# Performance work log

Measured on AMD Instinct MI355X. Metric: run time of the kernel, lower is better.

Reference implementation:

```python
import jax, jax.numpy as jnp
import numpy as np

B, N, NEMBED, E, H = 4, 256, 10000, 63, 128
D = E + 1  # feature dim after concat = 64


def _lin(key, fan_in, fan_out):
    k1, k2 = jax.random.split(key)
    bound = 1.0 / np.sqrt(fan_in)
    W = jax.random.uniform(k1, (fan_in, fan_out), jnp.float32, -bound, bound)
    b = jax.random.uniform(k2, (fan_out,), jnp.float32, -bound, bound)
    return W, b


def setup_inputs() -> dict:
    key = jax.random.key(0)
    ks = jax.random.split(key, 9)
    xcat = jax.random.randint(ks[0], (B, N), 0, NEMBED, dtype=jnp.int64)
    xfeat = jax.random.normal(ks[1], (B, N), dtype=jnp.float32)
    emb = jax.random.normal(ks[2], (NEMBED, E), dtype=jnp.float32)
    W1, b1 = _lin(ks[3], D, H)
    W2, b2 = _lin(ks[4], H, H)
    W3, b3 = _lin(ks[5], H, H)
    D1, c1 = _lin(ks[6], H, H)
    D2, c2 = _lin(ks[7], H, H)
    D3, c3 = _lin(ks[8], H, 1)
    return {"xcat": xcat, "xfeat": xfeat, "emb": emb,
            "W1": W1, "b1": b1, "W2": W2, "b2": b2, "W3": W3, "b3": b3,
            "D1": D1, "c1": c1, "D2": D2, "c2": c2, "D3": D3, "c3": c3}


def reference(xcat, xfeat, emb, W1, b1, W2, b2, W3, b3, D1, c1, D2, c2, D3, c3):
    # embed + concat scalar feature -> [B, N, D]
    x = jnp.concatenate([emb[xcat], xfeat[..., None]], axis=-1)
    # pairwise outer product over the set dim -> [B, N, N, D]
    # (original: einsum 'bid,bjd->bdij' then permute(0,2,3,1) == 'bid,bjd->bijd')
    p = jnp.einsum('bid,bjd->bijd', x, x)
    # per-pair 3-layer MLP (enc)
    h = jnp.maximum(p @ W1 + b1, 0.0)
    h = jnp.maximum(h @ W2 + b2, 0.0)
    h = h @ W3 + b3
    # relu -> mean pool over (i, j) -> relu; dropout is identity in eval
    h = jnp.maximum(h, 0.0)
    h = jnp.mean(h, axis=(1, 2))  # [B, H]
    h = jnp.maximum(h, 0.0)
    # dec MLP -> [B, 1]
    h = jnp.maximum(h @ D1 + c1, 0.0)
    h = jnp.maximum(h @ D2 + c2, 0.0)
    return h @ D3 + c3
```

## Files before the change

### kernel.cpp

```cpp
#include <hip/hip_runtime.h>
#include <hip/hip_bf16.h>


#define NB 4
#define NN 256
#define HD 128
#define TPB 257

typedef __attribute__((ext_vector_type(8))) short bf16x8;
typedef __attribute__((ext_vector_type(4))) float f32x4;

__device__ __forceinline__ unsigned rne2(float a, float b) {
    unsigned ua = __builtin_bit_cast(unsigned, a);
    unsigned ub = __builtin_bit_cast(unsigned, b);
    ua = ua + 0x7fff + ((ua >> 16) & 1);
    ub = ub + 0x7fff + ((ub >> 16) & 1);
    return (ua >> 16) | (ub & 0xffff0000u);
}

__device__ __forceinline__ short f2bf(float f) {
    unsigned u = __builtin_bit_cast(unsigned, f);
    u = (u + 0x7fff + ((u >> 16) & 1)) >> 16;
    return (short)u;
}

__device__ __forceinline__ void tri_ij(int t, int& i, int& j) {
    j = (int)((sqrtf(8.0f * (float)t + 1.0f) - 1.0f) * 0.5f);
    while (((j + 1) * (j + 2) >> 1) <= t) ++j;
    while (((j * (j + 1)) >> 1) > t) --j;
    i = t - ((j * (j + 1)) >> 1);
}

__device__ __forceinline__ void pack_w_nat(const float* __restrict__ W, short* __restrict__ pw,
                                           int KQ, int u) {
    int l  = u & 63;
    int kq = (u >> 6) % KQ;
    int mt = (u >> 6) / KQ;
    int q = l >> 4, m = l & 15;
    int c = mt * 16 + m;
#pragma unroll
    for (int j = 0; j < 8; ++j) {
        int k = kq * 32 + q * 8 + j;
        pw[u * 8 + j] = f2bf(W[k * 128 + c]);
    }
}

__device__ __forceinline__ void pack_w_perm(const float* __restrict__ W, short* __restrict__ pw,
                                            int u) {
    int l  = u & 63;
    int kq = (u >> 6) & 3;
    int mt = (u >> 6) >> 2;
    int q = l >> 4, m = l & 15;
    int c = mt * 16 + m;
#pragma unroll
    for (int j = 0; j < 8; ++j) {
        int k = 32 * kq + 16 * (j >> 2) + 4 * q + (j & 3);
        pw[u * 8 + j] = f2bf(W[k * 128 + c]);
    }
}

__global__ void prep_kernel(const int* __restrict__ xcat,
                            const float* __restrict__ xfeat,
                            const float* __restrict__ emb,
                            const float* __restrict__ W1,
                            const float* __restrict__ W2,
                            const float* __restrict__ W3,
                            float* __restrict__ x,
                            short* __restrict__ pw1,
                            short* __restrict__ pw2,
                            short* __restrict__ pw3)
{
    int bid = blockIdx.x;
    int tid = threadIdx.x;
    if (bid < 256) {
        int f = bid * 256 + tid;
        int d = f & 63;
        int nn = f >> 6;
        float v;
        if (d < 63) v = emb[xcat[nn] * 63 + d];
        else        v = xfeat[nn];
        x[f] = v;
    } else if (bid < 260) {
        pack_w_nat(W1, pw1, 2, (bid - 256) * 256 + tid);
    } else if (bid < 268) {
        pack_w_perm(W2, pw2, (bid - 260) * 256 + tid);
    } else {
        pack_w_perm(W3, pw3, (bid - 268) * 256 + tid);
    }
}

__global__ __launch_bounds__(256, 3) void pair_mlp(
    const float* __restrict__ x,
    const short* __restrict__ pw1, const float* __restrict__ b1,
    const short* __restrict__ pw2, const float* __restrict__ b2,
    const short* __restrict__ pw3, const float* __restrict__ b3,
    float* __restrict__ partialOut)
{
    __shared__ float smPart[4][HD];

    const int tid = threadIdx.x;
    const int w = __builtin_amdgcn_readfirstlane(tid >> 6);
    const int l = tid & 63;
    const int q = l >> 4;
    const int n = l & 15;
    const int b = blockIdx.y;
    const float* xb = x + (b << 14);

    const int p0 = blockIdx.x * 128 + w * 32 + n;
    int i0, j0, i1, j1;
    tri_ij(p0, i0, j0);
    tri_ij(p0 + 16, i1, j1);
    const float wp0 = (i0 == j0) ? 1.0f : 2.0f;
    const float wp1 = (i1 == j1) ? 1.0f : 2.0f;

    bf16x8 bp[2][2];
    {
        const float* xi[2] = {xb + (i0 << 6), xb + (i1 << 6)};
        const float* xj[2] = {xb + (j0 << 6), xb + (j1 << 6)};
#pragma unroll
        for (int nt = 0; nt < 2; ++nt)
#pragma unroll
            for (int kq = 0; kq < 2; ++kq) {
                int dd = kq * 32 + q * 8;
                float4 A0 = *(const float4*)(xi[nt] + dd);
                float4 A1 = *(const float4*)(xi[nt] + dd + 4);
                float4 B0 = *(const float4*)(xj[nt] + dd);
                float4 B1 = *(const float4*)(xj[nt] + dd + 4);
                uint4 s;
                s.x = rne2(A0.x * B0.x, A0.y * B0.y);
                s.y = rne2(A0.z * B0.z, A0.w * B0.w);
                s.z = rne2(A1.x * B1.x, A1.y * B1.y);
                s.w = rne2(A1.z * B1.z, A1.w * B1.w);
                bp[nt][kq] = __builtin_bit_cast(bf16x8, s);
            }
    }

    f32x4 acc[8][2];
    unsigned pk[2][8][2];

#pragma unroll
    for (int mt = 0; mt < 8; ++mt) {
        float4 bv = *(const float4*)(b1 + mt * 16 + q * 4);
        f32x4 init = {bv.x, bv.y, bv.z, bv.w};
        acc[mt][0] = init; acc[mt][1] = init;
    }
#pragma unroll
    for (int kq = 0; kq < 2; ++kq)
#pragma unroll
        for (int mt = 0; mt < 8; ++mt) {
            bf16x8 afr = *(const bf16x8*)(pw1 + (((mt * 2 + kq) * 64 + l) << 3));
            acc[mt][0] = __builtin_amdgcn_mfma_f32_16x16x32_bf16(afr, bp[0][kq], acc[mt][0], 0, 0, 0);
            acc[mt][1] = __builtin_amdgcn_mfma_f32_16x16x32_bf16(afr, bp[1][kq], acc[mt][1], 0, 0, 0);
        }

#pragma unroll
    for (int nt = 0; nt < 2; ++nt)
#pragma unroll
        for (int mt = 0; mt < 8; ++mt) {
            pk[nt][mt][0] = rne2(fmaxf(acc[mt][nt][0], 0.f), fmaxf(acc[mt][nt][1], 0.f));
            pk[nt][mt][1] = rne2(fmaxf(acc[mt][nt][2], 0.f), fmaxf(acc[mt][nt][3], 0.f));
        }

#pragma unroll
    for (int mt = 0; mt < 8; ++mt) {
        float4 bv = *(const float4*)(b2 + mt * 16 + q * 4);
        f32x4 init = {bv.x, bv.y, bv.z, bv.w};
        acc[mt][0] = init; acc[mt][1] = init;
    }
#pragma unroll
    for (int kq = 0; kq < 4; ++kq) {
        uint4 u0 = {pk[0][2 * kq][0], pk[0][2 * kq][1], pk[0][2 * kq + 1][0], pk[0][2 * kq + 1][1]};
        uint4 u1 = {pk[1][2 * kq][0], pk[1][2 * kq][1], pk[1][2 * kq + 1][0], pk[1][2 * kq + 1][1]};
        bf16x8 bf0 = __builtin_bit_cast(bf16x8, u0);
        bf16x8 bf1 = __builtin_bit_cast(bf16x8, u1);
#pragma unroll
        for (int mt = 0; mt < 8; ++mt) {
            bf16x8 afr = *(const bf16x8*)(pw2 + (((mt * 4 + kq) * 64 + l) << 3));
            acc[mt][0] = __builtin_amdgcn_mfma_f32_16x16x32_bf16(afr, bf0, acc[mt][0], 0, 0, 0);
            acc[mt][1] = __builtin_amdgcn_mfma_f32_16x16x32_bf16(afr, bf1, acc[mt][1], 0, 0, 0);
        }
    }

#pragma unroll
    for (int nt = 0; nt < 2; ++nt)
#pragma unroll
        for (int mt = 0; mt < 8; ++mt) {
            pk[nt][mt][0] = rne2(fmaxf(acc[mt][nt][0], 0.f), fmaxf(acc[mt][nt][1], 0.f));
            pk[nt][mt][1] = rne2(fmaxf(acc[mt][nt][2], 0.f), fmaxf(acc[mt][nt][3], 0.f));
        }

#pragma unroll
    for (int mt = 0; mt < 8; ++mt) {
        float4 bv = *(const float4*)(b3 + mt * 16 + q * 4);
        f32x4 init = {bv.x, bv.y, bv.z, bv.w};
        acc[mt][0] = init; acc[mt][1] = init;
    }
#pragma unroll
    for (int kq = 0; kq < 4; ++kq) {
        uint4 u0 = {pk[0][2 * kq][0], pk[0][2 * kq][1], pk[0][2 * kq + 1][0], pk[0][2 * kq + 1][1]};
        uint4 u1 = {pk[1][2 * kq][0], pk[1][2 * kq][1], pk[1][2 * kq + 1][0], pk[1][2 * kq + 1][1]};
        bf16x8 bf0 = __builtin_bit_cast(bf16x8, u0);
        bf16x8 bf1 = __builtin_bit_cast(bf16x8, u1);
#pragma unroll
        for (int mt = 0; mt < 8; ++mt) {
            bf16x8 afr = *(const bf16x8*)(pw3 + (((mt * 4 + kq) * 64 + l) << 3));
            acc[mt][0] = __builtin_amdgcn_mfma_f32_16x16x32_bf16(afr, bf0, acc[mt][0], 0, 0, 0);
            acc[mt][1] = __builtin_amdgcn_mfma_f32_16x16x32_bf16(afr, bf1, acc[mt][1], 0, 0, 0);
        }
    }

#pragma unroll
    for (int mt = 0; mt < 8; ++mt) {
        float vs[4];
#pragma unroll
        for (int r = 0; r < 4; ++r) {
            float v = wp0 * fmaxf(acc[mt][0][r], 0.f) + wp1 * fmaxf(acc[mt][1][r], 0.f);
            v += __shfl_xor(v, 1, 64);
            v += __shfl_xor(v, 2, 64);
            v += __shfl_xor(v, 4, 64);
            v += __shfl_xor(v, 8, 64);
            vs[r] = v;
        }
        if (n == 0) {
            float4 o = {vs[0], vs[1], vs[2], vs[3]};
            *(float4*)(&smPart[w][mt * 16 + q * 4]) = o;
        }
    }
    __syncthreads();

    if (tid < HD) {
        float v = (smPart[0][tid] + smPart[1][tid]) + (smPart[2][tid] + smPart[3][tid]);
        partialOut[(b * TPB + blockIdx.x) * HD + tid] = v;
    }
}

__global__ __launch_bounds__(1024) void reduce_decode(
    const float* __restrict__ partial,
    const float* __restrict__ D1, const float* __restrict__ c1,
    const float* __restrict__ D2, const float* __restrict__ c2,
    const float* __restrict__ D3, const float* __restrict__ c3,
    float* __restrict__ out)
{
    __shared__ float red8[8][HD];
    __shared__ float red2[2][HD];
    __shared__ float hb[HD];
    __shared__ float tb[HD];
    const int b = blockIdx.x;
    const int t = threadIdx.x;
    const int ch = t & 127, sl = t >> 7;

    {
        const float* base = partial + b * TPB * HD + ch;
        float s0 = 0.f, s1 = 0.f, s2 = 0.f, s3 = 0.f;
        int tl = sl;
        for (; tl + 32 <= TPB; tl += 32) {
            s0 += base[(tl     ) * HD];
            s1 += base[(tl +  8) * HD];
            s2 += base[(tl + 16) * HD];
            s3 += base[(tl + 24) * HD];
        }
        for (; tl < TPB; tl += 8) s0 += base[tl * HD];
        red8[sl][ch] = (s0 + s1) + (s2 + s3);
    }
    __syncthreads();
    if (sl == 0) {
        float v = ((red8[0][ch] + red8[1][ch]) + (red8[2][ch] + red8[3][ch]))
                + ((red8[4][ch] + red8[5][ch]) + (red8[6][ch] + red8[7][ch]));
        hb[ch] = fmaxf(v * (1.0f / 65536.0f), 0.0f);
    }
    __syncthreads();

    const int hf = sl & 1;

    if (t < 256) {
        float a = 0.f;
        for (int k = hf * 64; k < hf * 64 + 64; ++k)
            a = fmaf(hb[k], D1[(k << 7) + ch], a);
        red2[hf][ch] = a;
    }
    __syncthreads();
    if (t < 128)
        tb[ch] = fmaxf(red2[0][ch] + red2[1][ch] + c1[ch], 0.0f);
    __syncthreads();

    if (t < 256) {
        float a = 0.f;
        for (int k = hf * 64; k < hf * 64 + 64; ++k)
            a = fmaf(tb[k], D2[(k << 7) + ch], a);
        red2[hf][ch] = a;
    }
    __syncthreads();
    if (t < 128)
        hb[ch] = fmaxf(red2[0][ch] + red2[1][ch] + c2[ch], 0.0f);
    __syncthreads();

    if (t < 128) red2[0][ch] = hb[ch] * D3[ch];
    __syncthreads();
    if (t < 64) {
        float r = red2[0][t] + red2[0][t + 64];
#pragma unroll
        for (int s2 = 1; s2 < 64; s2 <<= 1)
            r += __shfl_xor(r, s2, 64);
        if (t == 0) out[b] = r + c3[0];
    }
}

extern "C" void kernel_launch(void* const* d_in, const int* in_sizes, int n_in,
                              void* d_out, int out_size, void* d_ws, size_t ws_size,
                              hipStream_t stream)
{
    (void)in_sizes; (void)n_in; (void)out_size; (void)ws_size;

    const int*   xcat  = (const int*)  d_in[0];
    const float* xfeat = (const float*)d_in[1];
    const float* emb   = (const float*)d_in[2];
    const float* W1    = (const float*)d_in[3];
    const float* b1    = (const float*)d_in[4];
    const float* W2    = (const float*)d_in[5];
    const float* b2    = (const float*)d_in[6];
    const float* W3    = (const float*)d_in[7];
    const float* b3    = (const float*)d_in[8];
    const float* D1    = (const float*)d_in[9];
    const float* c1    = (const float*)d_in[10];
    const float* D2    = (const float*)d_in[11];
    const float* c2    = (const float*)d_in[12];
    const float* D3    = (const float*)d_in[13];
    const float* c3    = (const float*)d_in[14];
    float* out = (float*)d_out;

    float* x       = (float*)d_ws;
    short* pw1     = (short*)(x + NB * NN * 64);
    short* pw2     = pw1 + 8 * 2 * 64 * 8;
    short* pw3     = pw2 + 8 * 4 * 64 * 8;
    float* partial = (float*)(pw3 + 8 * 4 * 64 * 8);

    prep_kernel<<<276, 256, 0, stream>>>(xcat, xfeat, emb, W1, W2, W3,
                                         x, pw1, pw2, pw3);
    pair_mlp<<<dim3(TPB, NB), 256, 0, stream>>>(x, pw1, b1, pw2, b2, pw3, b3, partial);
    reduce_decode<<<NB, 1024, 0, stream>>>(partial, D1, c1, D2, c2, D3, c3, out);
}
```

Baseline: 131.4 us.

## Stage MLP weights in LDS and widen pair tiles per wave

The pair-MLP kernel now uses 512-thread blocks, each handling 512 pairs, with each wave processing 64 pairs (four 16-column tiles) instead of 32. At block start, all three packed weight matrices are staged into 64 KB of shared memory, with W3 double-buffered into the W1 slot after layer 1, so MFMA A-fragments come from LDS instead of repeated global loads. Out-of-range pairs in the last block are clamped and given zero weight. Per-wave partial sums go straight to global memory and the reduce kernel reads more rows. This trades fewer global weight reads and better weight reuse for much higher register pressure (32 accumulators per lane), a grid of only 260 blocks, and extra block-wide barriers.

```diff
diff --git a/kernel.cpp b/kernel.cpp
--- a/kernel.cpp
+++ b/kernel.cpp
@@ -5,7 +5,8 @@
 #define NB 4
 #define NN 256
 #define HD 128
-#define TPB 257
+#define BPB 65
+#define NPAIR 32896
 
 typedef __attribute__((ext_vector_type(8))) short bf16x8;
 typedef __attribute__((ext_vector_type(4))) float f32x4;
@@ -89,14 +90,14 @@
     }
 }
 
-__global__ __launch_bounds__(256, 3) void pair_mlp(
+__global__ __launch_bounds__(512, 2) void pair_mlp(
     const float* __restrict__ x,
-    const short* __restrict__ pw1, const float* __restrict__ b1,
-    const short* __restrict__ pw2, const float* __restrict__ b2,
-    const short* __restrict__ pw3, const float* __restrict__ b3,
+    const short* __restrict__ pw1g, const float* __restrict__ b1,
+    const short* __restrict__ pw2g, const float* __restrict__ b2,
+    const short* __restrict__ pw3g, const float* __restrict__ b3,
     float* __restrict__ partialOut)
 {
-    __shared__ float smPart[4][HD];
+    __shared__ __align__(16) short smW[32768];
 
     const int tid = threadIdx.x;
     const int w = __builtin_amdgcn_readfirstlane(tid >> 6);
@@ -106,115 +107,160 @@
     const int b = blockIdx.y;
     const float* xb = x + (b << 14);
 
-    const int p0 = blockIdx.x * 128 + w * 32 + n;
-    int i0, j0, i1, j1;
-    tri_ij(p0, i0, j0);
-    tri_ij(p0 + 16, i1, j1);
-    const float wp0 = (i0 == j0) ? 1.0f : 2.0f;
-    const float wp1 = (i1 == j1) ? 1.0f : 2.0f;
-
-    bf16x8 bp[2][2];
+    float4* H0w = (float4*)smW;
+    float4* H1w = (float4*)(smW + 16384);
+    const float4* s1 = (const float4*)pw1g;
+    const float4* s2 = (const float4*)pw2g;
+    const float4* s3 = (const float4*)pw3g;
+    float4 g3[4];
     {
-        const float* xi[2] = {xb + (i0 << 6), xb + (i1 << 6)};
-        const float* xj[2] = {xb + (j0 << 6), xb + (j1 << 6)};
-#pragma unroll
-        for (int nt = 0; nt < 2; ++nt)
-#pragma unroll
-            for (int kq = 0; kq < 2; ++kq) {
-                int dd = kq * 32 + q * 8;
-                float4 A0 = *(const float4*)(xi[nt] + dd);
-                float4 A1 = *(const float4*)(xi[nt] + dd + 4);
-                float4 B0 = *(const float4*)(xj[nt] + dd);
-                float4 B1 = *(const float4*)(xj[nt] + dd + 4);
-                uint4 s;
-                s.x = rne2(A0.x * B0.x, A0.y * B0.y);
-                s.y = rne2(A0.z * B0.z, A0.w * B0.w);
-                s.z = rne2(A1.x * B1.x, A1.y * B1.y);
-                s.w = rne2(A1.z * B1.z, A1.w * B1.w);
-                bp[nt][kq] = __builtin_bit_cast(bf16x8, s);
-            }
-    }
-
-    f32x4 acc[8][2];
-    unsigned pk[2][8][2];
+        float4 g1a = s1[tid], g1b = s1[tid + 512];
+        float4 g2[4];
+#pragma unroll
+        for (int k = 0; k < 4; ++k) g2[k] = s2[tid + 512 * k];
+#pragma unroll
+        for (int k = 0; k < 4; ++k) g3[k] = s3[tid + 512 * k];
+        H0w[tid] = g1a; H0w[tid + 512] = g1b;
+#pragma unroll
+        for (int k = 0; k < 4; ++k) H1w[tid + 512 * k] = g2[k];
+    }
+
+    const int base = blockIdx.x * 512 + w * 64 + n;
+    int iv[4], jv[4];
+    float wp[4];
+#pragma unroll
+    for (int nt = 0; nt < 4; ++nt) {
+        int praw = base + nt * 16;
+        int pc = praw <= (NPAIR - 1) ? praw : (NPAIR - 1);
+        tri_ij(pc, iv[nt], jv[nt]);
+        wp[nt] = (praw <= (NPAIR - 1)) ? ((iv[nt] == jv[nt]) ? 1.0f : 2.0f) : 0.0f;
+    }
+
+    bf16x8 bp[4][2];
+#pragma unroll
+    for (int nt = 0; nt < 4; ++nt) {
+        const float* xi = xb + (iv[nt] << 6);
+        const float* xj = xb + (jv[nt] << 6);
+#pragma unroll
+        for (int kq = 0; kq < 2; ++kq) {
+            int dd = kq * 32 + q * 8;
+            float4 A0 = *(const float4*)(xi + dd);
+            float4 A1 = *(const float4*)(xi + dd + 4);
+            float4 B0 = *(const float4*)(xj + dd);
+            float4 B1 = *(const float4*)(xj + dd + 4);
+            uint4 s;
+            s.x = rne2(A0.x * B0.x, A0.y * B0.y);
+            s.y = rne2(A0.z * B0.z, A0.w * B0.w);
+            s.z = rne2(A1.x * B1.x, A1.y * B1.y);
+            s.w = rne2(A1.z * B1.z, A1.w * B1.w);
+            bp[nt][kq] = __builtin_bit_cast(bf16x8, s);
+        }
+    }
+    __syncthreads();
+
+    const bf16x8* F0 = (const bf16x8*)smW;
+    const bf16x8* F1 = (const bf16x8*)(smW + 16384);
+
+    f32x4 acc[8][4];
+    unsigned pk[4][8][2];
 
 #pragma unroll
     for (int mt = 0; mt < 8; ++mt) {
         float4 bv = *(const float4*)(b1 + mt * 16 + q * 4);
         f32x4 init = {bv.x, bv.y, bv.z, bv.w};
-        acc[mt][0] = init; acc[mt][1] = init;
+#pragma unroll
+        for (int nt = 0; nt < 4; ++nt) acc[mt][nt] = init;
     }
 #pragma unroll
     for (int kq = 0; kq < 2; ++kq)
 #pragma unroll
         for (int mt = 0; mt < 8; ++mt) {
-            bf16x8 afr = *(const bf16x8*)(pw1 + (((mt * 2 + kq) * 64 + l) << 3));
-            acc[mt][0] = __builtin_amdgcn_mfma_f32_16x16x32_bf16(afr, bp[0][kq], acc[mt][0], 0, 0, 0);
-            acc[mt][1] = __builtin_amdgcn_mfma_f32_16x16x32_bf16(afr, bp[1][kq], acc[mt][1], 0, 0, 0);
-        }
-
-#pragma unroll
-    for (int nt = 0; nt < 2; ++nt)
+            bf16x8 afr = F0[(mt * 2 + kq) * 64 + l];
+#pragma unroll
+            for (int nt = 0; nt < 4; ++nt)
+                acc[mt][nt] = __builtin_amdgcn_mfma_f32_16x16x32_bf16(afr, bp[nt][kq], acc[mt][nt], 0, 0, 0);
+        }
+
+#pragma unroll
+    for (int nt = 0; nt < 4; ++nt)
 #pragma unroll
         for (int mt = 0; mt < 8; ++mt) {
             pk[nt][mt][0] = rne2(fmaxf(acc[mt][nt][0], 0.f), fmaxf(acc[mt][nt][1], 0.f));
             pk[nt][mt][1] = rne2(fmaxf(acc[mt][nt][2], 0.f), fmaxf(acc[mt][nt][3], 0.f));
         }
+
+    __syncthreads();
+    H0w[tid] = g3[0]; H0w[tid + 512] = g3[1];
+    H0w[tid + 1024] = g3[2]; H0w[tid + 1536] = g3[3];
 
 #pragma unroll
     for (int mt = 0; mt < 8; ++mt) {
         float4 bv = *(const float4*)(b2 + mt * 16 + q * 4);
         f32x4 init = {bv.x, bv.y, bv.z, bv.w};
-        acc[mt][0] = init; acc[mt][1] = init;
+#pragma unroll
+        for (int nt = 0; nt < 4; ++nt) acc[mt][nt] = init;
     }
 #pragma unroll
     for (int kq = 0; kq < 4; ++kq) {
-        uint4 u0 = {pk[0][2 * kq][0], pk[0][2 * kq][1], pk[0][2 * kq + 1][0], pk[0][2 * kq + 1][1]};
-        uint4 u1 = {pk[1][2 * kq][0], pk[1][2 * kq][1], pk[1][2 * kq + 1][0], pk[1][2 * kq + 1][1]};
-        bf16x8 bf0 = __builtin_bit_cast(bf16x8, u0);
-        bf16x8 bf1 = __builtin_bit_cast(bf16x8, u1);
-#pragma unroll
-        for (int mt = 0; mt < 8; ++mt) {
-            bf16x8 afr = *(const bf16x8*)(pw2 + (((mt * 4 + kq) * 64 + l) << 3));
-            acc[mt][0] = __builtin_amdgcn_mfma_f32_16x16x32_bf16(afr, bf0, acc[mt][0], 0, 0, 0);
-            acc[mt][1] = __builtin_amdgcn_mfma_f32_16x16x32_bf16(afr, bf1, acc[mt][1], 0, 0, 0);
-        }
-    }
-
-#pragma unroll
-    for (int nt = 0; nt < 2; ++nt)
+        bf16x8 bf[4];
+#pragma unroll
+        for (int nt = 0; nt < 4; ++nt) {
+            uint4 u = {pk[nt][2 * kq][0], pk[nt][2 * kq][1],
+                       pk[nt][2 * kq + 1][0], pk[nt][2 * kq + 1][1]};
+            bf[nt] = __builtin_bit_cast(bf16x8, u);
+        }
+#pragma unroll
+        for (int mt = 0; mt < 8; ++mt) {
+            bf16x8 afr = F1[(mt * 4 + kq) * 64 + l];
+#pragma unroll
+            for (int nt = 0; nt < 4; ++nt)
+                acc[mt][nt] = __builtin_amdgcn_mfma_f32_16x16x32_bf16(afr, bf[nt], acc[mt][nt], 0, 0, 0);
+        }
+    }
+
+#pragma unroll
+    for (int nt = 0; nt < 4; ++nt)
 #pragma unroll
         for (int mt = 0; mt < 8; ++mt) {
             pk[nt][mt][0] = rne2(fmaxf(acc[mt][nt][0], 0.f), fmaxf(acc[mt][nt][1], 0.f));
             pk[nt][mt][1] = rne2(fmaxf(acc[mt][nt][2], 0.f), fmaxf(acc[mt][nt][3], 0.f));
         }
+
+    __syncthreads();
 
 #pragma unroll
     for (int mt = 0; mt < 8; ++mt) {
         float4 bv = *(const float4*)(b3 + mt * 16 + q * 4);
         f32x4 init = {bv.x, bv.y, bv.z, bv.w};
-        acc[mt][0] = init; acc[mt][1] = init;
+#pragma unroll
+        for (int nt = 0; nt < 4; ++nt) acc[mt][nt] = init;
     }
 #pragma unroll
     for (int kq = 0; kq < 4; ++kq) {
-        uint4 u0 = {pk[0][2 * kq][0], pk[0][2 * kq][1], pk[0][2 * kq + 1][0], pk[0][2 * kq + 1][1]};
-        uint4 u1 = {pk[1][2 * kq][0], pk[1][2 * kq][1], pk[1][2 * kq + 1][0], pk[1][2 * kq + 1][1]};
-        bf16x8 bf0 = __builtin_bit_cast(bf16x8, u0);
-        bf16x8 bf1 = __builtin_bit_cast(bf16x8, u1);
-#pragma unroll
-        for (int mt = 0; mt < 8; ++mt) {
-            bf16x8 afr = *(const bf16x8*)(pw3 + (((mt * 4 + kq) * 64 + l) << 3));
-            acc[mt][0] = __builtin_amdgcn_mfma_f32_16x16x32_bf16(afr, bf0, acc[mt][0], 0, 0, 0);
-            acc[mt][1] = __builtin_amdgcn_mfma_f32_16x16x32_bf16(afr, bf1, acc[mt][1], 0, 0, 0);
-        }
-    }
-
+        bf16x8 bf[4];
+#pragma unroll
+        for (int nt = 0; nt < 4; ++nt) {
+            uint4 u = {pk[nt][2 * kq][0], pk[nt][2 * kq][1],
+                       pk[nt][2 * kq + 1][0], pk[nt][2 * kq + 1][1]};
+            bf[nt] = __builtin_bit_cast(bf16x8, u);
+        }
+#pragma unroll
+        for (int mt = 0; mt < 8; ++mt) {
+            bf16x8 afr = F0[(mt * 4 + kq) * 64 + l];
+#pragma unroll
+            for (int nt = 0; nt < 4; ++nt)
+                acc[mt][nt] = __builtin_amdgcn_mfma_f32_16x16x32_bf16(afr, bf[nt], acc[mt][nt], 0, 0, 0);
+        }
+    }
+
+    const int row = (b * BPB + blockIdx.x) * 8 + w;
 #pragma unroll
     for (int mt = 0; mt < 8; ++mt) {
         float vs[4];
 #pragma unroll
         for (int r = 0; r < 4; ++r) {
-            float v = wp0 * fmaxf(acc[mt][0][r], 0.f) + wp1 * fmaxf(acc[mt][1][r], 0.f);
+            float v = wp[0] * fmaxf(acc[mt][0][r], 0.f) + wp[1] * fmaxf(acc[mt][1][r], 0.f)
+                    + wp[2] * fmaxf(acc[mt][2][r], 0.f) + wp[3] * fmaxf(acc[mt][3][r], 0.f);
             v += __shfl_xor(v, 1, 64);
             v += __shfl_xor(v, 2, 64);
             v += __shfl_xor(v, 4, 64);
@@ -223,17 +269,12 @@
         }
         if (n == 0) {
             float4 o = {vs[0], vs[1], vs[2], vs[3]};
-            *(float4*)(&smPart[w][mt * 16 + q * 4]) = o;
-        }
-    }
-    __syncthreads();
-
-    if (tid < HD) {
-        float v = (smPart[0][tid] + smPart[1][tid]) + (smPart[2][tid] + smPart[3][tid]);
-        partialOut[(b * TPB + blockIdx.x) * HD + tid] = v;
-    }
-}
-
+            *(float4*)(partialOut + row * HD + mt * 16 + q * 4) = o;
+        }
+    }
+}
+
+#define RROWS (BPB * 8)
 __global__ __launch_bounds__(1024) void reduce_decode(
     const float* __restrict__ partial,
     const float* __restrict__ D1, const float* __restrict__ c1,
@@ -250,16 +291,16 @@
     const int ch = t & 127, sl = t >> 7;
 
     {
-        const float* base = partial + b * TPB * HD + ch;
+        const float* base = partial + b * RROWS * HD + ch;
         float s0 = 0.f, s1 = 0.f, s2 = 0.f, s3 = 0.f;
         int tl = sl;
-        for (; tl + 32 <= TPB; tl += 32) {
+        for (; tl + 32 <= RROWS; tl += 32) {
             s0 += base[(tl     ) * HD];
             s1 += base[(tl +  8) * HD];
             s2 += base[(tl + 16) * HD];
             s3 += base[(tl + 24) * HD];
         }
-        for (; tl < TPB; tl += 8) s0 += base[tl * HD];
+        for (; tl < RROWS; tl += 8) s0 += base[tl * HD];
         red8[sl][ch] = (s0 + s1) + (s2 + s3);
     }
     __syncthreads();
@@ -336,6 +377,6 @@
 
     prep_kernel<<<276, 256, 0, stream>>>(xcat, xfeat, emb, W1, W2, W3,
                                          x, pw1, pw2, pw3);
-    pair_mlp<<<dim3(TPB, NB), 256, 0, stream>>>(x, pw1, b1, pw2, b2, pw3, b3, partial);
+    pair_mlp<<<dim3(BPB, NB), 512, 0, stream>>>(x, pw1, b1, pw2, b2, pw3, b3, partial);
     reduce_decode<<<NB, 1024, 0, stream>>>(partial, D1, c1, D2, c2, D3, c3, out);
 }
```

After: 131.0 us. About the same (-0.3%).
